# Kernel tuning notes

Measured on AMD Instinct MI355X. Metric: run time of the kernel, lower is better.

The kernel has to match this reference:

```python
import jax, jax.numpy as jnp
import numpy as np

D_MODEL = 1024
STATE_DIM = 64
SEQ_L = 2048


def hippo_legs_A(N):
    n = jnp.arange(N, dtype=jnp.float32)
    two_n1 = 2.0 * n + 1.0
    sq = jnp.sqrt(two_n1[:, None] * two_n1[None, :])
    A = jnp.tril(sq, k=-1) * -1.0
    return A + jnp.diag(-(n + 1.0))


def setup_inputs() -> dict:
    key = jax.random.key(0)
    kB, kC = jax.random.split(key)
    N = STATE_DIM
    n = jnp.arange(N, dtype=jnp.float32)
    B_ref = jnp.sqrt(2.0 * n + 1.0)  # (N,)
    B = jnp.tile(B_ref[None, :], (D_MODEL, 1)) + 0.01 * jax.random.normal(kB, (D_MODEL, N), dtype=jnp.float32)
    C = 0.1 * jax.random.normal(kC, (D_MODEL, N), dtype=jnp.float32)
    D = jnp.zeros((D_MODEL,), dtype=jnp.float32)
    log_dt = jnp.log(jnp.asarray(0.1, dtype=jnp.float32))
    return {"B": B, "C": C, "D": D, "log_dt": log_dt, "L": SEQ_L}


def reference(B, C, D, log_dt, L):
    N = B.shape[1]
    A = hippo_legs_A(N)                       # (N,N) continuous-time HiPPO-LegS
    dt = jax.nn.softplus(log_dt) + 1e-06
    I = jnp.eye(N, dtype=A.dtype)
    lhs = I - 0.5 * dt * A
    rhs = I + 0.5 * dt * A
    A_bar = jnp.linalg.solve(lhs, rhs)        # (N,N) bilinear discretization
    B_bar = jnp.linalg.solve(lhs, (dt * B).T).T  # (d_model, N)
    A_bar_T = A_bar.T

    def step(x, _):
        y = jnp.sum(C * x, axis=-1)           # (d_model,)
        return x @ A_bar_T, y

    _, ys = jax.lax.scan(step, B_bar, None, length=L)  # ys: (L, d_model)
    K = ys.T                                   # (d_model, L)
    K = K.at[:, 0].add(D)
    return K[:, None, :]                       # (d_model, 1, L)
```

## Files before the change

kernel.cpp:

```cpp
#include <hip/hip_runtime.h>

namespace {

template<int CTRL, int RM>
__device__ __forceinline__ float dpp_mov0(float v) {
  return __int_as_float(__builtin_amdgcn_update_dpp(
      0, __float_as_int(v), CTRL, RM, 0xF, false));
}
template<int CTRL, int RM>
__device__ __forceinline__ float dpp_mov1(float v) {
  return __int_as_float(__builtin_amdgcn_update_dpp(
      0x3f800000, __float_as_int(v), CTRL, RM, 0xF, false));
}

__device__ __forceinline__ float rl(float v, int k) {
  return __int_as_float(__builtin_amdgcn_readlane(__float_as_int(v), k));
}

struct Hoist {
  float cs0, cs1, cs2, cs3, cs4, cs5;
  float gs0, gs1, gs2, gs3, gs4, gs5;
  float r, inv_d, hr, alpha, k2;
};

__device__ __forceinline__ Hoist make_hoist(float dt, int n) {
  float h = 0.5f * dt, fn = (float)n;
  float r = sqrtf(2.f * fn + 1.f);
  float d = 1.f + h * (fn + 1.f);
  float inv_d = 1.f / d;
  float g = (1.f - h * fn) * inv_d;
  float c = g - 1.f;
  Hoist H;
  H.r = r; H.inv_d = inv_d; H.hr = h * r;
  H.alpha = 1.f + h * fn;
  H.k2 = r * (2.f - d) * inv_d;
#define COEF_STEP(IDX, CTRL, RM)                                        \
  H.cs##IDX = c; H.gs##IDX = g;                                         \
  { float cP = dpp_mov0<CTRL, RM>(c);                                   \
    float gP = dpp_mov1<CTRL, RM>(g);                                   \
    c = fmaf(g, cP, c); g = g * gP; }
  COEF_STEP(0, 0x111, 0xF)
  COEF_STEP(1, 0x112, 0xF)
  COEF_STEP(2, 0x114, 0xF)
  COEF_STEP(3, 0x118, 0xF)
  COEF_STEP(4, 0x142, 0xA)
  COEF_STEP(5, 0x143, 0xC)
#undef COEF_STEP
  return H;
}

__device__ __forceinline__ float abar_apply(float x, const Hoist& H) {
  float w1 = H.r * x, w2 = H.k2 * x;
#define APPLY_STEP(IDX, CTRL, RM)                                       \
  { float w1P = dpp_mov0<CTRL, RM>(w1);                                 \
    float w2P = dpp_mov0<CTRL, RM>(w2);                                 \
    w2 = fmaf(H.cs##IDX, w1P, fmaf(H.gs##IDX, w2P, w2));                \
    w1 += w1P; }
  APPLY_STEP(0, 0x111, 0xF)
  APPLY_STEP(1, 0x112, 0xF)
  APPLY_STEP(2, 0x114, 0xF)
  APPLY_STEP(3, 0x118, 0xF)
  APPLY_STEP(4, 0x142, 0xA)
  APPLY_STEP(5, 0x143, 0xC)
#undef APPLY_STEP
  float tp = dpp_mov0<0x138, 0xF>(w2);
  return H.inv_d * fmaf(-H.hr, w1 + tp, H.alpha * x);
}

template<int CTRL, int RM>
__device__ __forceinline__ void linrec_step(float& G, float& W) {
  float Wo = dpp_mov0<CTRL, RM>(W);
  float Go = dpp_mov1<CTRL, RM>(G);
  W = fmaf(G, Wo, W);
  G *= Go;
}
__device__ __forceinline__ float lhs_solve(float z, const Hoist& H) {
  float G = H.gs0, W = H.r * z * H.inv_d;
  linrec_step<0x111, 0xF>(G, W);
  linrec_step<0x112, 0xF>(G, W);
  linrec_step<0x114, 0xF>(G, W);
  linrec_step<0x118, 0xF>(G, W);
  linrec_step<0x142, 0xA>(G, W);
  linrec_step<0x143, 0xC>(G, W);
  float sp = dpp_mov0<0x138, 0xF>(W);
  return (z - H.hr * sp) * H.inv_d;
}

__device__ __forceinline__ float softplus_dt(float ldt) {
  return log1pf(expf(ldt)) + 1e-6f;
}

__device__ __forceinline__ void load_row_g(const float* __restrict__ base,
                                           float (&pc)[64]) {
  const float4* p4 = (const float4*)base;
  #pragma unroll
  for (int q = 0; q < 16; ++q) {
    float4 f = p4[q];
    pc[4*q+0] = f.x; pc[4*q+1] = f.y; pc[4*q+2] = f.z; pc[4*q+3] = f.w;
  }
}

__device__ __forceinline__ float qapply(const float (&pc)[64], float u) {
  float a0 = 0.f, a1 = 0.f, a2 = 0.f, a3 = 0.f;
  #pragma unroll
  for (int k = 0; k < 64; k += 4) {
    a0 = fmaf(pc[k + 0], rl(u, k + 0), a0);
    a1 = fmaf(pc[k + 1], rl(u, k + 1), a1);
    a2 = fmaf(pc[k + 2], rl(u, k + 2), a2);
    a3 = fmaf(pc[k + 3], rl(u, k + 3), a3);
  }
  return (a0 + a1) + (a2 + a3);
}

__device__ __forceinline__ float grow_matvec(const float* __restrict__ M,
                                             float u, int lane) {
  float a0 = 0.f, a1 = 0.f, a2 = 0.f, a3 = 0.f;
  const float4* m4 = (const float4*)(M + lane * 64);
  #pragma unroll
  for (int q = 0; q < 16; ++q) {
    float4 f = m4[q];
    a0 = fmaf(f.x, rl(u, 4 * q + 0), a0);
    a1 = fmaf(f.y, rl(u, 4 * q + 1), a1);
    a2 = fmaf(f.z, rl(u, 4 * q + 2), a2);
    a3 = fmaf(f.w, rl(u, 4 * q + 3), a3);
  }
  return (a0 + a1) + (a2 + a3);
}

__device__ __forceinline__ int vidx(int j, int n) {
  return j * 64 + ((((n >> 2) ^ (j & 15)) << 2) | (n & 3));
}

}

__global__ __launch_bounds__(64) void hippo_pow(const float* __restrict__ ldt_p,
                                                float* __restrict__ A32c,
                                                float* __restrict__ QROW) {
  const int lane = threadIdx.x;
  const int m = blockIdx.x;
  const float dt = softplus_dt(ldt_p[0]);
  const Hoist H = make_hoist(dt, lane);
  float x = (lane == m) ? 1.f : 0.f;
  #pragma unroll 1
  for (int s = 0; s < 32; ++s) x = abar_apply(x, H);
  A32c[lane * 64 + m] = x;
  #pragma unroll 1
  for (int s = 0; s < 32; ++s) x = abar_apply(x, H);
  QROW[m * 64 + lane] = x;
}

__global__ __launch_bounds__(256, 2) void hippo_main(
    const float* __restrict__ B, const float* __restrict__ C,
    const float* __restrict__ Dv, const float* __restrict__ ldt_p,
    const float* __restrict__ A32c, const float* __restrict__ QROW,
    float* __restrict__ out, int NI, int L) {
  __shared__ __align__(16) float Vl[64 * 64];
  __shared__ __align__(16) float Ul[32 * 64];
  const int d = blockIdx.x;
  const int tau = threadIdx.x;
  const int lane = tau & 63;
  const int w = tau >> 6;
  const int role = (w + d) & 3;
  const float dt = softplus_dt(ldt_p[0]);

  if (role == 0) {
    const Hoist H = make_hoist(dt, lane);
    float v = lhs_solve(dt * B[d * 64 + lane], H);
    #pragma unroll 1
    for (int j = 0; j < 32; ++j) {
      Vl[vidx(j, lane)] = v;
      if (j < 31) v = abar_apply(v, H);
    }
  } else if (role == 3) {
    const Hoist H = make_hoist(dt, lane);
    float bb = lhs_solve(dt * B[d * 64 + lane], H);
    float v = grow_matvec(A32c, bb, lane);
    #pragma unroll 1
    for (int j = 32; j < 64; ++j) {
      Vl[vidx(j, lane)] = v;
      if (j < 63) v = abar_apply(v, H);
    }
  } else if (role == 1) {
    float pc[64];
    load_row_g(QROW + lane * 64, pc);
    float u = C[d * 64 + lane];
    #pragma unroll 1
    for (int i = 0; i < NI; ++i) {
      Ul[i * 64 + lane] = u;
      if (i < NI - 1) u = qapply(pc, u);
    }
  }
  __syncthreads();

  const int j = lane;
  float ureg[8];
  #pragma unroll
  for (int k = 0; k < 8; ++k) {
    const int i = w + 4 * k;
    ureg[k] = (i < NI) ? Ul[i * 64 + lane] : 0.f;
  }
  float acc[8];
  #pragma unroll
  for (int k = 0; k < 8; ++k) acc[k] = 0.f;
  #pragma unroll
  for (int h = 0; h < 4; ++h) {
    float vr[16];
    #pragma unroll
    for (int q4 = 0; q4 < 4; ++q4) {
      const int q = h * 4 + q4;
      float4 f = *(const float4*)&Vl[j * 64 + ((q ^ (j & 15)) << 2)];
      vr[4*q4+0] = f.x; vr[4*q4+1] = f.y; vr[4*q4+2] = f.z; vr[4*q4+3] = f.w;
    }
    #pragma unroll
    for (int k = 0; k < 8; ++k) {
      #pragma unroll
      for (int e = 0; e < 16; ++e) {
        acc[k] = fmaf(vr[e], rl(ureg[k], 16 * h + e), acc[k]);
      }
    }
  }
  #pragma unroll
  for (int k = 0; k < 8; ++k) {
    const int i = w + 4 * k;
    if (i < NI) {
      float y = acc[k];
      if ((i | j) == 0) y += Dv[d];
      out[(size_t)d * L + i * 64 + j] = y;
    }
  }
}

extern "C" void kernel_launch(void* const* d_in, const int* in_sizes, int n_in,
                              void* d_out, int out_size, void* d_ws, size_t ws_size,
                              hipStream_t stream) {
  const float* B   = (const float*)d_in[0];
  const float* C   = (const float*)d_in[1];
  const float* Dv  = (const float*)d_in[2];
  const float* ldt = (const float*)d_in[3];
  const int d_model = in_sizes[2];
  const int L = out_size / d_model;
  const int NI = L / 64;
  float* A32c = (float*)d_ws;
  float* QROW = (float*)d_ws + 4096;
  hippo_pow<<<64, 64, 0, stream>>>(ldt, A32c, QROW);
  hippo_main<<<1024, 256, 0, stream>>>(B, C, Dv, ldt, A32c, QROW,
                                       (float*)d_out, NI, L);
}
```

Before: 43.68 us.

## Split main kernel into chain-generation and epilogue kernels via global workspace

The fused per-row kernel is split into two launches. The first runs only the three sequential chain wavefronts (V halves and U powers) in 192-thread blocks and writes V and U to a global workspace. The second reloads V into swizzled LDS and does the matmul epilogue with all four waves. The aim is to stop the idle fourth wave from holding block resources during the serial chains and to let each phase get its own occupancy. The cost is an extra launch plus a roughly 24 MB global write and read round-trip.

```diff
diff --git a/kernel.cpp b/kernel.cpp
--- a/kernel.cpp
+++ b/kernel.cpp
@@ -127,10 +127,6 @@
   return (a0 + a1) + (a2 + a3);
 }
 
-__device__ __forceinline__ int vidx(int j, int n) {
-  return j * 64 + ((((n >> 2) ^ (j & 15)) << 2) | (n & 3));
-}
-
 }
 
 __global__ __launch_bounds__(64) void hippo_pow(const float* __restrict__ ldt_p,
@@ -149,46 +145,65 @@
   QROW[m * 64 + lane] = x;
 }
 
-__global__ __launch_bounds__(256, 2) void hippo_main(
+__global__ __launch_bounds__(192) void hippo_chains(
     const float* __restrict__ B, const float* __restrict__ C,
-    const float* __restrict__ Dv, const float* __restrict__ ldt_p,
-    const float* __restrict__ A32c, const float* __restrict__ QROW,
-    float* __restrict__ out, int NI, int L) {
-  __shared__ __align__(16) float Vl[64 * 64];
-  __shared__ __align__(16) float Ul[32 * 64];
+    const float* __restrict__ ldt_p, const float* __restrict__ A32c,
+    const float* __restrict__ QROW, float* __restrict__ Vg,
+    float* __restrict__ Ug, int NI) {
   const int d = blockIdx.x;
   const int tau = threadIdx.x;
   const int lane = tau & 63;
   const int w = tau >> 6;
-  const int role = (w + d) & 3;
   const float dt = softplus_dt(ldt_p[0]);
-
-  if (role == 0) {
+  float* Vd = Vg + (size_t)d * 4096;
+  float* Ud = Ug + (size_t)d * 2048;
+
+  if (w == 0) {
     const Hoist H = make_hoist(dt, lane);
     float v = lhs_solve(dt * B[d * 64 + lane], H);
     #pragma unroll 1
     for (int j = 0; j < 32; ++j) {
-      Vl[vidx(j, lane)] = v;
+      Vd[j * 64 + lane] = v;
       if (j < 31) v = abar_apply(v, H);
     }
-  } else if (role == 3) {
+  } else if (w == 1) {
     const Hoist H = make_hoist(dt, lane);
     float bb = lhs_solve(dt * B[d * 64 + lane], H);
     float v = grow_matvec(A32c, bb, lane);
     #pragma unroll 1
     for (int j = 32; j < 64; ++j) {
-      Vl[vidx(j, lane)] = v;
+      Vd[j * 64 + lane] = v;
       if (j < 63) v = abar_apply(v, H);
     }
-  } else if (role == 1) {
+  } else {
     float pc[64];
     load_row_g(QROW + lane * 64, pc);
     float u = C[d * 64 + lane];
     #pragma unroll 1
     for (int i = 0; i < NI; ++i) {
-      Ul[i * 64 + lane] = u;
+      Ud[i * 64 + lane] = u;
       if (i < NI - 1) u = qapply(pc, u);
     }
+  }
+}
+
+__global__ __launch_bounds__(256) void hippo_epi(
+    const float* __restrict__ Dv, const float* __restrict__ Vg,
+    const float* __restrict__ Ug, float* __restrict__ out, int NI, int L) {
+  __shared__ __align__(16) float Vl[64 * 64];
+  const int d = blockIdx.x;
+  const int tau = threadIdx.x;
+  const int lane = tau & 63;
+  const int w = tau >> 6;
+  const float* Vd = Vg + (size_t)d * 4096;
+  const float* Ud = Ug + (size_t)d * 2048;
+
+  #pragma unroll
+  for (int p = 0; p < 4; ++p) {
+    const int idx = tau + 256 * p;
+    const int j = idx >> 4, q = idx & 15;
+    float4 f = *(const float4*)(Vd + idx * 4);
+    *(float4*)&Vl[j * 64 + ((q ^ (j & 15)) << 2)] = f;
   }
   __syncthreads();
 
@@ -197,7 +212,7 @@
   #pragma unroll
   for (int k = 0; k < 8; ++k) {
     const int i = w + 4 * k;
-    ureg[k] = (i < NI) ? Ul[i * 64 + lane] : 0.f;
+    ureg[k] = (i < NI) ? Ud[i * 64 + lane] : 0.f;
   }
   float acc[8];
   #pragma unroll
@@ -242,7 +257,9 @@
   const int NI = L / 64;
   float* A32c = (float*)d_ws;
   float* QROW = (float*)d_ws + 4096;
+  float* Vg   = (float*)d_ws + 8192;
+  float* Ug   = Vg + (size_t)d_model * 4096;
   hippo_pow<<<64, 64, 0, stream>>>(ldt, A32c, QROW);
-  hippo_main<<<1024, 256, 0, stream>>>(B, C, Dv, ldt, A32c, QROW,
-                                       (float*)d_out, NI, L);
-}
+  hippo_chains<<<d_model, 192, 0, stream>>>(B, C, ldt, A32c, QROW, Vg, Ug, NI);
+  hippo_epi<<<d_model, 256, 0, stream>>>(Dv, Vg, Ug, (float*)d_out, NI, L);
+}
```

New measurement: 51.24 us. 17.3% more time.

## Use split-bf16 MFMA for output product and parallelize U recurrence across two waves

Applied to the files above, without the earlier changes.

The final U·V product, formerly scalar FMAs with readlane broadcasts, now runs on bf16 MFMA 16x16x32 instructions. Each fp32 value is split into a high and low bf16 pair and three MFMAs per tile approximate fp32 accuracy. The serial C-side recurrence of 32 steps is split across two waves, each stepping by A^64 (a new Q2ROW precomputed in hippo_pow) over 16 steps. The rotating wave-role assignment is dropped. This adds extra pow-kernel work, some precision loss from dropping the lo*lo term, and hardcodes L=2048 in the output indexing.

```diff
diff --git a/kernel.cpp b/kernel.cpp
--- a/kernel.cpp
+++ b/kernel.cpp
@@ -1,4 +1,9 @@
 #include <hip/hip_runtime.h>
+
+typedef unsigned short ushort_t;
+typedef unsigned int uint_t;
+typedef short short8 __attribute__((ext_vector_type(8)));
+typedef float f32x4 __attribute__((ext_vector_type(4)));
 
 namespace {
 
@@ -127,15 +132,26 @@
   return (a0 + a1) + (a2 + a3);
 }
 
-__device__ __forceinline__ int vidx(int j, int n) {
-  return j * 64 + ((((n >> 2) ^ (j & 15)) << 2) | (n & 3));
+__device__ __forceinline__ void split_store(float v, ushort_t* Hi,
+                                            ushort_t* Lo, int row, int n) {
+  uint_t uv = __float_as_uint(v);
+  float hf = __uint_as_float(uv & 0xFFFF0000u);
+  uint_t lv = __float_as_uint(v - hf);
+  int idx = (row << 6) | (((n >> 3) ^ (row & 7)) << 3) | (n & 7);
+  Hi[idx] = (ushort_t)(uv >> 16);
+  Lo[idx] = (ushort_t)(lv >> 16);
+}
+
+__device__ __forceinline__ int frag_off(int row, int chunk) {
+  return (row << 6) | ((chunk ^ (row & 7)) << 3);
 }
 
 }
 
 __global__ __launch_bounds__(64) void hippo_pow(const float* __restrict__ ldt_p,
                                                 float* __restrict__ A32c,
-                                                float* __restrict__ QROW) {
+                                                float* __restrict__ QROW,
+                                                float* __restrict__ Q2ROW) {
   const int lane = threadIdx.x;
   const int m = blockIdx.x;
   const float dt = softplus_dt(ldt_p[0]);
@@ -147,86 +163,96 @@
   #pragma unroll 1
   for (int s = 0; s < 32; ++s) x = abar_apply(x, H);
   QROW[m * 64 + lane] = x;
+  #pragma unroll 1
+  for (int s = 0; s < 64; ++s) x = abar_apply(x, H);
+  Q2ROW[m * 64 + lane] = x;
 }
 
 __global__ __launch_bounds__(256, 2) void hippo_main(
     const float* __restrict__ B, const float* __restrict__ C,
     const float* __restrict__ Dv, const float* __restrict__ ldt_p,
     const float* __restrict__ A32c, const float* __restrict__ QROW,
-    float* __restrict__ out, int NI, int L) {
-  __shared__ __align__(16) float Vl[64 * 64];
-  __shared__ __align__(16) float Ul[32 * 64];
+    const float* __restrict__ Q2ROW, float* __restrict__ out,
+    int NI, int L) {
+  __shared__ __align__(16) ushort_t Uh[32 * 64], Ulo[32 * 64];
+  __shared__ __align__(16) ushort_t Vh[64 * 64], Vlo[64 * 64];
   const int d = blockIdx.x;
   const int tau = threadIdx.x;
   const int lane = tau & 63;
   const int w = tau >> 6;
-  const int role = (w + d) & 3;
   const float dt = softplus_dt(ldt_p[0]);
 
-  if (role == 0) {
+  if (w == 0) {
     const Hoist H = make_hoist(dt, lane);
     float v = lhs_solve(dt * B[d * 64 + lane], H);
     #pragma unroll 1
     for (int j = 0; j < 32; ++j) {
-      Vl[vidx(j, lane)] = v;
+      split_store(v, Vh, Vlo, j, lane);
       if (j < 31) v = abar_apply(v, H);
     }
-  } else if (role == 3) {
+  } else if (w == 3) {
     const Hoist H = make_hoist(dt, lane);
     float bb = lhs_solve(dt * B[d * 64 + lane], H);
     float v = grow_matvec(A32c, bb, lane);
     #pragma unroll 1
     for (int j = 32; j < 64; ++j) {
-      Vl[vidx(j, lane)] = v;
+      split_store(v, Vh, Vlo, j, lane);
       if (j < 63) v = abar_apply(v, H);
     }
-  } else if (role == 1) {
+  } else if (w == 1) {
     float pc[64];
-    load_row_g(QROW + lane * 64, pc);
+    load_row_g(Q2ROW + lane * 64, pc);
     float u = C[d * 64 + lane];
     #pragma unroll 1
-    for (int i = 0; i < NI; ++i) {
-      Ul[i * 64 + lane] = u;
-      if (i < NI - 1) u = qapply(pc, u);
+    for (int a = 0; a < 16; ++a) {
+      split_store(u, Uh, Ulo, 2 * a, lane);
+      if (a < 15) u = qapply(pc, u);
+    }
+  } else {
+    float pc[64];
+    load_row_g(Q2ROW + lane * 64, pc);
+    float u = grow_matvec(QROW, C[d * 64 + lane], lane);
+    #pragma unroll 1
+    for (int a = 0; a < 16; ++a) {
+      split_store(u, Uh, Ulo, 2 * a + 1, lane);
+      if (a < 15) u = qapply(pc, u);
     }
   }
   __syncthreads();
 
-  const int j = lane;
-  float ureg[8];
-  #pragma unroll
-  for (int k = 0; k < 8; ++k) {
-    const int i = w + 4 * k;
-    ureg[k] = (i < NI) ? Ul[i * 64 + lane] : 0.f;
-  }
-  float acc[8];
-  #pragma unroll
-  for (int k = 0; k < 8; ++k) acc[k] = 0.f;
-  #pragma unroll
-  for (int h = 0; h < 4; ++h) {
-    float vr[16];
-    #pragma unroll
-    for (int q4 = 0; q4 < 4; ++q4) {
-      const int q = h * 4 + q4;
-      float4 f = *(const float4*)&Vl[j * 64 + ((q ^ (j & 15)) << 2)];
-      vr[4*q4+0] = f.x; vr[4*q4+1] = f.y; vr[4*q4+2] = f.z; vr[4*q4+3] = f.w;
-    }
-    #pragma unroll
-    for (int k = 0; k < 8; ++k) {
-      #pragma unroll
-      for (int e = 0; e < 16; ++e) {
-        acc[k] = fmaf(vr[e], rl(ureg[k], 16 * h + e), acc[k]);
-      }
-    }
-  }
-  #pragma unroll
-  for (int k = 0; k < 8; ++k) {
-    const int i = w + 4 * k;
-    if (i < NI) {
-      float y = acc[k];
-      if ((i | j) == 0) y += Dv[d];
-      out[(size_t)d * L + i * 64 + j] = y;
-    }
+  const int it = w & 1;
+  const int jp = w >> 1;
+  const int arow = lane & 15;
+  const int kg = lane >> 4;
+  f32x4 acc0 = {0.f, 0.f, 0.f, 0.f};
+  f32x4 acc1 = {0.f, 0.f, 0.f, 0.f};
+  const int ia = (it << 4) + arow;
+  const int jv0 = (jp << 5) + arow;
+  const int jv1 = jv0 + 16;
+  #pragma unroll
+  for (int k0 = 0; k0 < 2; ++k0) {
+    const int ci = (k0 << 2) + kg;
+    short8 ah = *(const short8*)&Uh[frag_off(ia, ci)];
+    short8 al = *(const short8*)&Ulo[frag_off(ia, ci)];
+    short8 b0h = *(const short8*)&Vh[frag_off(jv0, ci)];
+    short8 b0l = *(const short8*)&Vlo[frag_off(jv0, ci)];
+    short8 b1h = *(const short8*)&Vh[frag_off(jv1, ci)];
+    short8 b1l = *(const short8*)&Vlo[frag_off(jv1, ci)];
+    acc0 = __builtin_amdgcn_mfma_f32_16x16x32_bf16(ah, b0h, acc0, 0, 0, 0);
+    acc0 = __builtin_amdgcn_mfma_f32_16x16x32_bf16(al, b0h, acc0, 0, 0, 0);
+    acc0 = __builtin_amdgcn_mfma_f32_16x16x32_bf16(ah, b0l, acc0, 0, 0, 0);
+    acc1 = __builtin_amdgcn_mfma_f32_16x16x32_bf16(ah, b1h, acc1, 0, 0, 0);
+    acc1 = __builtin_amdgcn_mfma_f32_16x16x32_bf16(al, b1h, acc1, 0, 0, 0);
+    acc1 = __builtin_amdgcn_mfma_f32_16x16x32_bf16(ah, b1l, acc1, 0, 0, 0);
+  }
+  #pragma unroll
+  for (int r = 0; r < 4; ++r) {
+    const int i = (it << 4) + (kg << 2) + r;
+    const int j0 = (jp << 5) + arow;
+    float y0 = acc0[r];
+    if (i == 0 && j0 == 0) y0 += Dv[d];
+    out[((size_t)d << 11) + (i << 6) + j0] = y0;
+    out[((size_t)d << 11) + (i << 6) + j0 + 16] = acc1[r];
   }
 }
 
@@ -240,9 +266,10 @@
   const int d_model = in_sizes[2];
   const int L = out_size / d_model;
   const int NI = L / 64;
-  float* A32c = (float*)d_ws;
-  float* QROW = (float*)d_ws + 4096;
-  hippo_pow<<<64, 64, 0, stream>>>(ldt, A32c, QROW);
-  hippo_main<<<1024, 256, 0, stream>>>(B, C, Dv, ldt, A32c, QROW,
-                                       (float*)d_out, NI, L);
-}
+  float* A32c  = (float*)d_ws;
+  float* QROW  = (float*)d_ws + 4096;
+  float* Q2ROW = (float*)d_ws + 8192;
+  hippo_pow<<<64, 64, 0, stream>>>(ldt, A32c, QROW, Q2ROW);
+  hippo_main<<<d_model, 256, 0, stream>>>(B, C, Dv, ldt, A32c, QROW, Q2ROW,
+                                          (float*)d_out, NI, L);
+}
```

Result: faster. 39.38 us (-9.9%).
